# Optimization experiments

Measured on AMD Instinct MI355X. Metric: run time of the kernel, lower is better.

The kernel has to match this reference:

```python
import jax, jax.numpy as jnp
import numpy as np

BETA = 1.0  # abs_model.beta


def setup_inputs() -> dict:
    key = jax.random.key(0)
    k1, k2, k3, k4 = jax.random.split(key, 4)
    B, C_img, H, W = 64, 3, 32, 32
    N, L, NC = 8000, 64, 10  # n_samples, n_latents, n_classes (one VAE per class)
    D = C_img * H * W
    x = jax.random.uniform(k1, (B, C_img, H, W), dtype=jnp.float32)
    z = jax.random.normal(k2, (N, L, 1, 1), dtype=jnp.float32)
    # per-class linear decoder weights (stand-in for vae.decoder); scaled so sigmoid is not saturated
    dec_w = jax.random.normal(k3, (NC, L, D), dtype=jnp.float32) * 0.05
    dec_b = jax.random.normal(k4, (NC, D), dtype=jnp.float32) * 0.05
    return {"x": x, "z": z, "dec_w": dec_w, "dec_b": dec_b}


def reference(x, z, dec_w, dec_b):
    B = x.shape[0]
    img_shape = x.shape[1:]
    NC, L, D = dec_w.shape
    N = z.shape[0]

    xf = x.reshape(B, D)                      # (B, D)
    zf = z.reshape(N, L)                      # (N, L)  -- mu == z, logvar == 0

    # KLD per candidate: -0.5 * sum(1 + logvar - mu^2 - exp(logvar)) with logvar=0
    kld = 0.5 * jnp.sum(zf * zf, axis=1)      # (N,)

    # decoders: rec = sigmoid(z @ W_c + b_c) for each class c
    recs = jax.nn.sigmoid(jnp.einsum('nl,cld->cnd', zf, dec_w) + dec_b[:, None, :])  # (NC, N, D)

    x_sq = jnp.sum(xf * xf, axis=1)           # (B,)
    r_sq = jnp.sum(recs * recs, axis=2)       # (NC, N)
    cross = jnp.einsum('bd,cnd->cbn', xf, recs)  # (NC, B, N)
    loss = x_sq[None, :, None] + r_sq[:, None, :] - 2.0 * cross + BETA * kld[None, None, :]

    losses = jnp.min(loss, axis=2)            # (NC, B)
    idx = jnp.argmin(loss, axis=2)            # (NC, B)

    recs_sel = jnp.take_along_axis(recs, idx[:, :, None], axis=1)  # (NC, B, D)
    recs_sel = recs_sel.reshape((NC, B) + img_shape)
    mus = zf[idx].reshape(NC, B, L, 1, 1)     # mu[indices] per vae, stacked

    logits = -losses.T                        # (B, NC)
    logvars = jnp.zeros_like(mus)
    return logits, recs_sel, mus, logvars
```

## Files before the change

### kernel.cpp

```cpp
#include <hip/hip_runtime.h>
#include <math.h>

#define B    64
#define D    3072
#define L    64
#define N    8000
#define NC   10
#define NT   64
#define DC   32
#define NBLK (N / NT)
#define NCH  (D / DC)

#define LOGITS_OFF 0
#define RECS_OFF   640
#define MUS_OFF    (640 + NC * B * D)
#define LV_OFF     (MUS_OFF + NC * B * L)

#define WSTG_OFF 0
#define XSTG_OFF 8847360
#define KLD_OFF  9633792
#define XSQ_OFF  9665792
#define PMIN_OFF 9666048
#define PIDX_OFF 9986048
#define FIDX_OFF 10306048

#define SCALE_UP   2048.0f
#define SCALE_DN   4.8828125e-4f

typedef __attribute__((ext_vector_type(8)))  _Float16 h16x8;
typedef __attribute__((ext_vector_type(16))) float    f32x16;

typedef const __attribute__((address_space(1))) unsigned int* gas1_t;
typedef __attribute__((address_space(3))) unsigned int*       las3_t;

#define MFMA16(a, b, c) __builtin_amdgcn_mfma_f32_32x32x16_f16(a, b, c, 0, 0, 0)

__device__ __forceinline__ unsigned pack2h(_Float16 lo, _Float16 hi) {
    union { _Float16 h[2]; unsigned u; } x;
    x.h[0] = lo; x.h[1] = hi;
    return x.u;
}

__global__ __launch_bounds__(256)
void prep_kernel(const float* __restrict__ xf, const float* __restrict__ zf,
                 const float* __restrict__ dw, const float* __restrict__ db,
                 unsigned short* __restrict__ Wstg, unsigned short* __restrict__ Xstg,
                 float* __restrict__ kld, float* __restrict__ xsq) {
    const int blk = blockIdx.x, t = threadIdx.x;
    if (blk < 960) {
        const int c = blk / 96, ch = blk % 96;
        __shared__ float wt[32][68];
        #pragma unroll
        for (int k = 0; k < 8; ++k) {
            int l = (t >> 5) + 8 * k;
            int d = t & 31;
            wt[d][l] = dw[(size_t)(c * 64 + l) * D + ch * 32 + d];
        }
        __syncthreads();
        const int d = t >> 3, lg = t & 7, l0 = lg * 8;
        float v[8];
        *(float4*)&v[0] = *(const float4*)&wt[d][l0];
        *(float4*)&v[4] = *(const float4*)&wt[d][l0 + 4];
        _Float16 p1[8], p2[8];
        #pragma unroll
        for (int j = 0; j < 8; ++j) {
            p1[j] = (_Float16)v[j];
            p2[j] = (_Float16)((v[j] - (float)p1[j]) * SCALE_UP);
        }
        unsigned short* reg = Wstg + (size_t)blk * 4608;
        *(uint4*)&reg[lg * 256 + d * 8]        = *(const uint4*)&p1[0];
        *(uint4*)&reg[2048 + lg * 256 + d * 8] = *(const uint4*)&p2[0];
        if (t < 32) ((float*)(reg + 4096))[t] = db[(size_t)c * D + ch * 32 + t];
    } else if (blk < 1056) {
        const int ch = blk - 960;
        const int b = t >> 2, dg = t & 3, dl0 = dg * 8;
        float v[8];
        *(float4*)&v[0] = *(const float4*)&xf[(size_t)b * D + ch * 32 + dl0];
        *(float4*)&v[4] = *(const float4*)&xf[(size_t)b * D + ch * 32 + dl0 + 4];
        _Float16 p1[8], p2[8];
        #pragma unroll
        for (int j = 0; j < 8; ++j) {
            p1[j] = (_Float16)v[j];
            p2[j] = (_Float16)((v[j] - (float)p1[j]) * SCALE_UP);
        }
        unsigned short* reg = Xstg + (size_t)ch * 4096;
        *(uint4*)&reg[dg * 512 + b * 8]        = *(const uint4*)&p1[0];
        *(uint4*)&reg[2048 + dg * 512 + b * 8] = *(const uint4*)&p2[0];
    } else if (blk < 1088) {
        int n = (blk - 1056) * 256 + t;
        if (n < N) {
            const float4* zp = (const float4*)(zf + (size_t)n * L);
            float s = 0.f;
            #pragma unroll
            for (int k = 0; k < 16; ++k) {
                float4 v4 = zp[k];
                s += v4.x * v4.x + v4.y * v4.y + v4.z * v4.z + v4.w * v4.w;
            }
            kld[n] = 0.5f * s;
        }
    } else {
        int b = blk - 1088;
        float s = 0.f;
        #pragma unroll
        for (int k = 0; k < 12; ++k) {
            float v = xf[(size_t)b * D + k * 256 + t];
            s = __builtin_fmaf(v, v, s);
        }
        for (int m = 1; m < 64; m <<= 1) s += __shfl_xor(s, m);
        __shared__ float ps[4];
        if ((t & 63) == 0) ps[t >> 6] = s;
        __syncthreads();
        if (t == 0) xsq[b] = ps[0] + ps[1] + ps[2] + ps[3];
    }
}

__global__ __launch_bounds__(128, 2)
void loss_kernel(const unsigned short* __restrict__ Wstg, const unsigned short* __restrict__ Xstg,
                 const float* __restrict__ zf, const float* __restrict__ kld,
                 const float* __restrict__ xsq,
                 float* __restrict__ pmin, int* __restrict__ pidx) {
    const int tid  = threadIdx.x;
    const int nh   = tid >> 6;
    const int lane = tid & 63;
    const int lrow = lane & 31;
    const int h    = lane >> 5;

    int bid = blockIdx.x;
    {
        int xcd = bid & 7, idx = bid >> 3;
        bid = (xcd < 2 ? xcd * 157 : 2 * 157 + (xcd - 2) * 156) + idx;
    }
    const int c  = bid / NBLK;
    const int nb = bid % NBLK;
    const int n0 = nb * NT;

    __shared__ __align__(16) unsigned char stg[2][17408];
    __shared__ float  xsq_s[B];
    __shared__ double vmin_s[2][B];
    __shared__ int    imin_s[2][B];

    h16x8 zfrag[4][2];
    {
        const float* zr = zf + (size_t)(n0 + 32 * nh + lrow) * L;
        #pragma unroll
        for (int ks = 0; ks < 4; ++ks) {
            float4 za = *(const float4*)(zr + ks * 16 + h * 8);
            float4 zb = *(const float4*)(zr + ks * 16 + h * 8 + 4);
            float vv[8] = {za.x, za.y, za.z, za.w, zb.x, zb.y, zb.z, zb.w};
            #pragma unroll
            for (int e = 0; e < 8; ++e) {
                _Float16 a1 = (_Float16)vv[e];
                zfrag[ks][0][e] = a1;
                zfrag[ks][1][e] = (_Float16)((vv[e] - (float)a1) * SCALE_UP);
            }
        }
    }
    if (tid < B) xsq_s[tid] = xsq[tid];

    const char* wsrc = (const char*)(Wstg + (size_t)(c * 96) * 4608);
    const char* xsrc = (const char*)Xstg;

#define STAGE(buf_, ch_)  do {                                                          \
        if (nh == 0) {                                                                  \
            const char* g_ = wsrc + (size_t)(ch_) * 9216 + lane * 16;                   \
            char* l_ = (char*)&stg[buf_][0];                                            \
            _Pragma("unroll")                                                           \
            for (int i_ = 0; i_ < 9; ++i_)                                              \
                __builtin_amdgcn_global_load_lds((gas1_t)(g_ + i_ * 1024),              \
                                                 (las3_t)(l_ + i_ * 1024), 16, 0, 0);   \
        } else {                                                                        \
            const char* g_ = xsrc + (size_t)(ch_) * 8192 + lane * 16;                   \
            char* l_ = (char*)&stg[buf_][9216];                                         \
            _Pragma("unroll")                                                           \
            for (int i_ = 0; i_ < 8; ++i_)                                              \
                __builtin_amdgcn_global_load_lds((gas1_t)(g_ + i_ * 1024),              \
                                                 (las3_t)(l_ + i_ * 1024), 16, 0, 0);   \
        } } while (0)

    int woff[4];
    #pragma unroll
    for (int ks = 0; ks < 4; ++ks)
        woff[ks] = (2 * ks + h) * 512 + lrow * 16;
    int xoff[2][2];
    #pragma unroll
    for (int bh = 0; bh < 2; ++bh)
        #pragma unroll
        for (int ks2 = 0; ks2 < 2; ++ks2)
            xoff[bh][ks2] = (2 * ks2 + h) * 1024 + (32 * bh + lrow) * 16;

    f32x16 acc2a = (f32x16)0.0f, acc2b = (f32x16)0.0f;
    f32x16 accca = (f32x16)0.0f, acccb = (f32x16)0.0f;
    f32x16 sh2a  = (f32x16)0.0f, sh2b  = (f32x16)0.0f;
    double racc_d = 0.0;

    STAGE(0, 0);
    __syncthreads();

    int buf = 0;
    for (int ch = 0; ch < NCH; ++ch) {
        if (ch + 1 < NCH) STAGE(buf ^ 1, ch + 1);

        const unsigned char* base = &stg[buf][0];

        f32x16 rt  = (f32x16)0.0f;
        f32x16 rtc = (f32x16)0.0f;
        #pragma unroll
        for (int ks = 0; ks < 4; ++ks) {
            h16x8 w1 = *(const h16x8*)(base + woff[ks]);
            h16x8 w2 = *(const h16x8*)(base + 4096 + woff[ks]);
            rt  = MFMA16(w1, zfrag[ks][0], rt);
            rtc = MFMA16(w1, zfrag[ks][1], rtc);
            rtc = MFMA16(w2, zfrag[ks][0], rtc);
        }

        const float* biasb = (const float*)(base + 8192);
        float4 bq[4];
        #pragma unroll
        for (int q = 0; q < 4; ++q) bq[q] = *(const float4*)&biasb[8 * q + 4 * h];

        float sv[16];
        float ch_r2 = 0.f;
        #pragma unroll
        for (int r_ = 0; r_ < 16; ++r_) {
            float a = __builtin_fmaf(rtc[r_], SCALE_DN, rt[r_]) + bq[r_ >> 2][r_ & 3];
            float r = __builtin_amdgcn_rcpf(1.0f + __expf(-a));
            sv[r_] = r;
            ch_r2 = __builtin_fmaf(r, r, ch_r2);
        }
        racc_d += (double)ch_r2;

        h16x8 rfrag[2];
        #pragma unroll
        for (int ks2 = 0; ks2 < 2; ++ks2) {
            _Float16 p1[8];
            #pragma unroll
            for (int e = 0; e < 8; ++e)
                p1[e] = (_Float16)sv[8 * ks2 + e];
            unsigned A0 = pack2h(p1[0], p1[1]), A1 = pack2h(p1[2], p1[3]);
            unsigned B0 = pack2h(p1[4], p1[5]), B1 = pack2h(p1[6], p1[7]);
            auto r02 = __builtin_amdgcn_permlane32_swap((int)A0, (int)B0, false, false);
            auto r13 = __builtin_amdgcn_permlane32_swap((int)A1, (int)B1, false, false);
            union { unsigned u[4]; h16x8 v; } f;
            f.u[0] = (unsigned)r02[0]; f.u[1] = (unsigned)r13[0];
            f.u[2] = (unsigned)r02[1]; f.u[3] = (unsigned)r13[1];
            rfrag[ks2] = f.v;
        }

        const unsigned char* xb = base + 9216;
        #pragma unroll
        for (int ks2 = 0; ks2 < 2; ++ks2) {
            h16x8 x1a = *(const h16x8*)(xb + xoff[0][ks2]);
            h16x8 x1b = *(const h16x8*)(xb + xoff[1][ks2]);
            h16x8 x2a = *(const h16x8*)(xb + 4096 + xoff[0][ks2]);
            h16x8 x2b = *(const h16x8*)(xb + 4096 + xoff[1][ks2]);
            acc2a = MFMA16(x1a, rfrag[ks2], acc2a);
            acc2b = MFMA16(x1b, rfrag[ks2], acc2b);
            accca = MFMA16(x2a, rfrag[ks2], accca);
            acccb = MFMA16(x2b, rfrag[ks2], acccb);
        }

        if ((ch & 31) == 31) {
            sh2a += acc2a; sh2b += acc2b;
            acc2a = (f32x16)0.0f; acc2b = (f32x16)0.0f;
        }

        __syncthreads();
        buf ^= 1;
    }
    sh2a += acc2a; sh2b += acc2b;

    double racc_t = racc_d + __shfl_xor(racc_d, 32);
    const int nglob = n0 + 32 * nh + lrow;
    const double rk = racc_t + (double)kld[nglob];

    double lv[2][16];
    int    bi[2][16];
    #pragma unroll
    for (int bh = 0; bh < 2; ++bh)
        #pragma unroll
        for (int r_ = 0; r_ < 16; ++r_) {
            int bb = 32 * bh + (r_ & 3) + 8 * (r_ >> 2) + 4 * h;
            double cr = (bh == 0)
                ? ((double)sh2a[r_] + (double)accca[r_] * (double)SCALE_DN)
                : ((double)sh2b[r_] + (double)acccb[r_] * (double)SCALE_DN);
            lv[bh][r_] = (double)xsq_s[bb] + rk - 2.0 * cr;
            bi[bh][r_] = nglob;
        }
    #pragma unroll
    for (int m = 1; m <= 16; m <<= 1) {
        #pragma unroll
        for (int bh = 0; bh < 2; ++bh)
            #pragma unroll
            for (int r_ = 0; r_ < 16; ++r_) {
                double ov = __shfl_xor(lv[bh][r_], m);
                int    oi = __shfl_xor(bi[bh][r_], m);
                if (ov < lv[bh][r_] || (ov == lv[bh][r_] && oi < bi[bh][r_])) {
                    lv[bh][r_] = ov; bi[bh][r_] = oi;
                }
            }
    }
    if (lrow == 0) {
        #pragma unroll
        for (int bh = 0; bh < 2; ++bh)
            #pragma unroll
            for (int r_ = 0; r_ < 16; ++r_) {
                int bb = 32 * bh + (r_ & 3) + 8 * (r_ >> 2) + 4 * h;
                vmin_s[nh][bb] = lv[bh][r_];
                imin_s[nh][bb] = bi[bh][r_];
            }
    }
    __syncthreads();
    if (tid < B) {
        double v0 = vmin_s[0][tid], v1 = vmin_s[1][tid];
        int    i0 = imin_s[0][tid], i1 = imin_s[1][tid];
        double bv; int bix;
        if (v1 < v0 || (v1 == v0 && i1 < i0)) { bv = v1; bix = i1; }
        else                                  { bv = v0; bix = i0; }
        pmin[((size_t)c * NBLK + nb) * B + tid] = (float)bv;
        pidx[((size_t)c * NBLK + nb) * B + tid] = bix;
    }
#undef STAGE
}

__global__ void reduce_kernel(const float* __restrict__ pmin, const int* __restrict__ pidx,
                              float* __restrict__ out, int* __restrict__ fidx) {
    int c = blockIdx.x, b = threadIdx.x;
    float bv = 3.4e38f; int bidx = 0x7fffffff;
    for (int nb = 0; nb < NBLK; ++nb) {
        float v = pmin[((size_t)c * NBLK + nb) * B + b];
        int   i = pidx[((size_t)c * NBLK + nb) * B + b];
        if (v < bv || (v == bv && i < bidx)) { bv = v; bidx = i; }
    }
    out[LOGITS_OFF + b * NC + c] = -bv;
    fidx[c * B + b] = bidx;
}

__global__ __launch_bounds__(256)
void final_kernel(const float* __restrict__ zf, const float* __restrict__ dw,
                  const float* __restrict__ db, const int* __restrict__ fidx,
                  float* __restrict__ out) {
    int c = blockIdx.x >> 6;
    int b = blockIdx.x & 63;
    int t = threadIdx.x;
    int n = fidx[c * B + b];
    __shared__ float zsh[64];
    if (t < 64) zsh[t] = zf[(size_t)n * L + t];
    __syncthreads();
    const float* wcc = dw + (size_t)c * L * D;
    float* rout = out + RECS_OFF + (size_t)(c * B + b) * D;
    for (int d = t; d < D; d += 256) {
        float a = db[(size_t)c * D + d];
        #pragma unroll 8
        for (int l = 0; l < L; ++l)
            a = __builtin_fmaf(zsh[l], wcc[(size_t)l * D + d], a);
        rout[d] = 1.0f / (1.0f + __expf(-a));
    }
    if (t < 64) {
        out[MUS_OFF + (size_t)(c * B + b) * L + t] = zsh[t];
        out[LV_OFF  + (size_t)(c * B + b) * L + t] = 0.0f;
    }
}

extern "C" void kernel_launch(void* const* d_in, const int* in_sizes, int n_in,
                              void* d_out, int out_size, void* d_ws, size_t ws_size,
                              hipStream_t stream) {
    const float* xf = (const float*)d_in[0];
    const float* zf = (const float*)d_in[1];
    const float* dw = (const float*)d_in[2];
    const float* db = (const float*)d_in[3];
    float* out = (float*)d_out;
    char* ws = (char*)d_ws;

    unsigned short* Wstg = (unsigned short*)(ws + WSTG_OFF);
    unsigned short* Xstg = (unsigned short*)(ws + XSTG_OFF);
    float* kld  = (float*)(ws + KLD_OFF);
    float* xsq  = (float*)(ws + XSQ_OFF);
    float* pmin = (float*)(ws + PMIN_OFF);
    int*   pidx = (int*)  (ws + PIDX_OFF);
    int*   fidx = (int*)  (ws + FIDX_OFF);

    hipLaunchKernelGGL(prep_kernel, dim3(1152), dim3(256), 0, stream,
                       xf, zf, dw, db, Wstg, Xstg, kld, xsq);
    hipLaunchKernelGGL(loss_kernel, dim3(NC * NBLK), dim3(128), 0, stream,
                       Wstg, Xstg, zf, kld, xsq, pmin, pidx);
    hipLaunchKernelGGL(reduce_kernel, dim3(NC), dim3(64), 0, stream, pmin, pidx, out, fidx);
    hipLaunchKernelGGL(final_kernel, dim3(NC * B), dim3(256), 0, stream, zf, dw, db, fidx, out);
}
```

Baseline: 422.6 us.

## Widen loss tiles to five waves, fold reduction into final kernel, vectorize decoder

The loss kernel now covers 160 candidates per block with five waves sharing each staged W/X chunk, instead of 64 candidates with two waves. This cuts redundant global/LDS staging per candidate and reduces the block count to 500, remapped across XCDs. The separate reduce kernel is removed, and the final kernel reduces the 50 partial minima itself with a wave shuffle. The final decoder loop is vectorized to float4. Fewer blocks (500) may underfill the GPU, and each block now runs more work in serial.

```diff
diff --git a/kernel.cpp b/kernel.cpp
--- a/kernel.cpp
+++ b/kernel.cpp
@@ -6,9 +6,10 @@
 #define L    64
 #define N    8000
 #define NC   10
-#define NT   64
+#define NT   160
+#define WV   5
 #define DC   32
-#define NBLK (N / NT)
+#define NBLKL (N / NT)
 #define NCH  (D / DC)
 
 #define LOGITS_OFF 0
@@ -22,7 +23,6 @@
 #define XSQ_OFF  9665792
 #define PMIN_OFF 9666048
 #define PIDX_OFF 9986048
-#define FIDX_OFF 10306048
 
 #define SCALE_UP   2048.0f
 #define SCALE_DN   4.8828125e-4f
@@ -114,13 +114,13 @@
     }
 }
 
-__global__ __launch_bounds__(128, 2)
+__global__ __launch_bounds__(320, 2)
 void loss_kernel(const unsigned short* __restrict__ Wstg, const unsigned short* __restrict__ Xstg,
                  const float* __restrict__ zf, const float* __restrict__ kld,
                  const float* __restrict__ xsq,
                  float* __restrict__ pmin, int* __restrict__ pidx) {
     const int tid  = threadIdx.x;
-    const int nh   = tid >> 6;
+    const int wid  = tid >> 6;
     const int lane = tid & 63;
     const int lrow = lane & 31;
     const int h    = lane >> 5;
@@ -128,20 +128,20 @@
     int bid = blockIdx.x;
     {
         int xcd = bid & 7, idx = bid >> 3;
-        bid = (xcd < 2 ? xcd * 157 : 2 * 157 + (xcd - 2) * 156) + idx;
-    }
-    const int c  = bid / NBLK;
-    const int nb = bid % NBLK;
+        bid = (xcd < 4 ? xcd * 63 : 252 + (xcd - 4) * 62) + idx;
+    }
+    const int c  = bid / NBLKL;
+    const int nb = bid % NBLKL;
     const int n0 = nb * NT;
 
     __shared__ __align__(16) unsigned char stg[2][17408];
     __shared__ float  xsq_s[B];
-    __shared__ double vmin_s[2][B];
-    __shared__ int    imin_s[2][B];
+    __shared__ double vmin_s[WV][B];
+    __shared__ int    imin_s[WV][B];
 
     h16x8 zfrag[4][2];
     {
-        const float* zr = zf + (size_t)(n0 + 32 * nh + lrow) * L;
+        const float* zr = zf + (size_t)(n0 + 32 * wid + lrow) * L;
         #pragma unroll
         for (int ks = 0; ks < 4; ++ks) {
             float4 za = *(const float4*)(zr + ks * 16 + h * 8);
@@ -161,14 +161,14 @@
     const char* xsrc = (const char*)Xstg;
 
 #define STAGE(buf_, ch_)  do {                                                          \
-        if (nh == 0) {                                                                  \
+        if (wid == 0) {                                                                 \
             const char* g_ = wsrc + (size_t)(ch_) * 9216 + lane * 16;                   \
             char* l_ = (char*)&stg[buf_][0];                                            \
             _Pragma("unroll")                                                           \
             for (int i_ = 0; i_ < 9; ++i_)                                              \
                 __builtin_amdgcn_global_load_lds((gas1_t)(g_ + i_ * 1024),              \
                                                  (las3_t)(l_ + i_ * 1024), 16, 0, 0);   \
-        } else {                                                                        \
+        } else if (wid == 1) {                                                          \
             const char* g_ = xsrc + (size_t)(ch_) * 8192 + lane * 16;                   \
             char* l_ = (char*)&stg[buf_][9216];                                         \
             _Pragma("unroll")                                                           \
@@ -270,7 +270,7 @@
     sh2a += acc2a; sh2b += acc2b;
 
     double racc_t = racc_d + __shfl_xor(racc_d, 32);
-    const int nglob = n0 + 32 * nh + lrow;
+    const int nglob = n0 + 32 * wid + lrow;
     const double rk = racc_t + (double)kld[nglob];
 
     double lv[2][16];
@@ -305,55 +305,81 @@
             #pragma unroll
             for (int r_ = 0; r_ < 16; ++r_) {
                 int bb = 32 * bh + (r_ & 3) + 8 * (r_ >> 2) + 4 * h;
-                vmin_s[nh][bb] = lv[bh][r_];
-                imin_s[nh][bb] = bi[bh][r_];
+                vmin_s[wid][bb] = lv[bh][r_];
+                imin_s[wid][bb] = bi[bh][r_];
             }
     }
     __syncthreads();
     if (tid < B) {
-        double v0 = vmin_s[0][tid], v1 = vmin_s[1][tid];
-        int    i0 = imin_s[0][tid], i1 = imin_s[1][tid];
-        double bv; int bix;
-        if (v1 < v0 || (v1 == v0 && i1 < i0)) { bv = v1; bix = i1; }
-        else                                  { bv = v0; bix = i0; }
-        pmin[((size_t)c * NBLK + nb) * B + tid] = (float)bv;
-        pidx[((size_t)c * NBLK + nb) * B + tid] = bix;
+        double bv = vmin_s[0][tid]; int bix = imin_s[0][tid];
+        #pragma unroll
+        for (int w = 1; w < WV; ++w) {
+            double v = vmin_s[w][tid]; int i = imin_s[w][tid];
+            if (v < bv || (v == bv && i < bix)) { bv = v; bix = i; }
+        }
+        pmin[((size_t)c * NBLKL + nb) * B + tid] = (float)bv;
+        pidx[((size_t)c * NBLKL + nb) * B + tid] = bix;
     }
 #undef STAGE
 }
 
-__global__ void reduce_kernel(const float* __restrict__ pmin, const int* __restrict__ pidx,
-                              float* __restrict__ out, int* __restrict__ fidx) {
-    int c = blockIdx.x, b = threadIdx.x;
-    float bv = 3.4e38f; int bidx = 0x7fffffff;
-    for (int nb = 0; nb < NBLK; ++nb) {
-        float v = pmin[((size_t)c * NBLK + nb) * B + b];
-        int   i = pidx[((size_t)c * NBLK + nb) * B + b];
-        if (v < bv || (v == bv && i < bidx)) { bv = v; bidx = i; }
-    }
-    out[LOGITS_OFF + b * NC + c] = -bv;
-    fidx[c * B + b] = bidx;
-}
-
 __global__ __launch_bounds__(256)
 void final_kernel(const float* __restrict__ zf, const float* __restrict__ dw,
-                  const float* __restrict__ db, const int* __restrict__ fidx,
-                  float* __restrict__ out) {
-    int c = blockIdx.x >> 6;
-    int b = blockIdx.x & 63;
-    int t = threadIdx.x;
-    int n = fidx[c * B + b];
+                  const float* __restrict__ db, const float* __restrict__ pmin,
+                  const int* __restrict__ pidx, float* __restrict__ out) {
+    const int c = blockIdx.x >> 6;
+    const int b = blockIdx.x & 63;
+    const int t = threadIdx.x;
+
+    __shared__ float pv[64];
+    __shared__ int   pi[64];
+    __shared__ int   nsel_s;
+    if (t < 64) {
+        if (t < NBLKL) {
+            pv[t] = pmin[((size_t)c * NBLKL + t) * B + b];
+            pi[t] = pidx[((size_t)c * NBLKL + t) * B + b];
+        } else { pv[t] = 3.4e38f; pi[t] = 0x7fffffff; }
+    }
+    __syncthreads();
+    if (t < 64) {
+        float v = pv[t]; int i = pi[t];
+        for (int m = 1; m < 64; m <<= 1) {
+            float ov = __shfl_xor(v, m);
+            int   oi = __shfl_xor(i, m);
+            if (ov < v || (ov == v && oi < i)) { v = ov; i = oi; }
+        }
+        if (t == 0) {
+            out[LOGITS_OFF + b * NC + c] = -v;
+            nsel_s = i;
+        }
+    }
+    __syncthreads();
+    const int n = nsel_s;
     __shared__ float zsh[64];
     if (t < 64) zsh[t] = zf[(size_t)n * L + t];
     __syncthreads();
+
     const float* wcc = dw + (size_t)c * L * D;
     float* rout = out + RECS_OFF + (size_t)(c * B + b) * D;
-    for (int d = t; d < D; d += 256) {
-        float a = db[(size_t)c * D + d];
-        #pragma unroll 8
-        for (int l = 0; l < L; ++l)
-            a = __builtin_fmaf(zsh[l], wcc[(size_t)l * D + d], a);
-        rout[d] = 1.0f / (1.0f + __expf(-a));
+    #pragma unroll
+    for (int k = 0; k < 3; ++k) {
+        const int d0 = (t + k * 256) * 4;
+        float4 a = *(const float4*)&db[(size_t)c * D + d0];
+        #pragma unroll 16
+        for (int l = 0; l < L; ++l) {
+            const float zl = zsh[l];
+            float4 w = *(const float4*)&wcc[(size_t)l * D + d0];
+            a.x = __builtin_fmaf(zl, w.x, a.x);
+            a.y = __builtin_fmaf(zl, w.y, a.y);
+            a.z = __builtin_fmaf(zl, w.z, a.z);
+            a.w = __builtin_fmaf(zl, w.w, a.w);
+        }
+        float4 r;
+        r.x = 1.0f / (1.0f + __expf(-a.x));
+        r.y = 1.0f / (1.0f + __expf(-a.y));
+        r.z = 1.0f / (1.0f + __expf(-a.z));
+        r.w = 1.0f / (1.0f + __expf(-a.w));
+        *(float4*)&rout[d0] = r;
     }
     if (t < 64) {
         out[MUS_OFF + (size_t)(c * B + b) * L + t] = zsh[t];
@@ -377,12 +403,11 @@
     float* xsq  = (float*)(ws + XSQ_OFF);
     float* pmin = (float*)(ws + PMIN_OFF);
     int*   pidx = (int*)  (ws + PIDX_OFF);
-    int*   fidx = (int*)  (ws + FIDX_OFF);
 
     hipLaunchKernelGGL(prep_kernel, dim3(1152), dim3(256), 0, stream,
                        xf, zf, dw, db, Wstg, Xstg, kld, xsq);
-    hipLaunchKernelGGL(loss_kernel, dim3(NC * NBLK), dim3(128), 0, stream,
+    hipLaunchKernelGGL(loss_kernel, dim3(NC * NBLKL), dim3(320), 0, stream,
                        Wstg, Xstg, zf, kld, xsq, pmin, pidx);
-    hipLaunchKernelGGL(reduce_kernel, dim3(NC), dim3(64), 0, stream, pmin, pidx, out, fidx);
-    hipLaunchKernelGGL(final_kernel, dim3(NC * B), dim3(256), 0, stream, zf, dw, db, fidx, out);
+    hipLaunchKernelGGL(final_kernel, dim3(NC * B), dim3(256), 0, stream,
+                       zf, dw, db, pmin, pidx, out);
 }
```

Measured after the change: 357.4 us. 15.4% less time.
